# Optimization experiments

Hardware: AMD Instinct MI355X
Metric: run time of the kernel (lower is better)

The kernel has to match this reference:

```python
import jax, jax.numpy as jnp
import numpy as np

SELU_SCALE = 1.0507009873554805
SELU_ALPHA = 1.6732632423543772

def _learned_activation(x, w):
    # softmax-blended mixture of 8 activations plus a zero 'linear' branch
    p = jax.nn.softmax(w)
    sig = jax.nn.sigmoid(x)
    elu = jax.nn.elu(x)
    tanh = jnp.tanh(x)
    relu = jax.nn.relu(x)
    silu = jax.nn.silu(x)
    gelu = jax.nn.gelu(x, approximate=False)
    selu = SELU_SCALE * jnp.where(x > 0, x, SELU_ALPHA * jnp.expm1(x))
    mish = x * jnp.tanh(jax.nn.softplus(x))
    return (p[0] * sig + p[1] * elu + p[2] * tanh + p[3] * relu
            + p[4] * silu + p[5] * gelu + p[6] * selu + p[7] * mish)  # p[8]*0 (linear=0)


def setup_inputs() -> dict:
    key = jax.random.key(0)
    ks = jax.random.split(key, 10)
    B, D, H, E, M = 1024, 1024, 2048, 8, 2048
    init_units = 1024
    s = lambda fan_in: 1.0 / np.sqrt(fan_in)
    x = jax.random.normal(ks[0], (B, D), jnp.float32)
    gate_w = jax.random.normal(ks[1], (D, E), jnp.float32) * s(D)
    expert_w = jax.random.normal(ks[2], (E, D, H), jnp.float32) * s(D)
    expert_b = jnp.zeros((E, H), jnp.float32)
    conn_w1 = jax.random.normal(ks[3], (E, H, 32), jnp.float32) * s(H)
    conn_b1 = jnp.zeros((E, 32), jnp.float32)
    conn_w2 = jax.random.normal(ks[4], (E, 32, H), jnp.float32) * s(32)
    conn_b2 = jnp.zeros((E, H), jnp.float32)
    neuron_avg = jax.random.uniform(ks[5], (E, H), jnp.float32)
    # initial mask: first initial_units neurons active per expert
    neuron_mask = jnp.tile(
        jnp.concatenate([jnp.ones((init_units,), jnp.float32),
                         jnp.zeros((H - init_units,), jnp.float32)])[None, :], (E, 1))
    mem_read_w = jax.random.normal(ks[6], (H, M), jnp.float32) * s(H)
    mem_read_b = jnp.zeros((M,), jnp.float32)
    memory = jax.random.normal(ks[7], (M, H), jnp.float32) * s(M)
    act_w = jnp.ones((9,), jnp.float32)
    return {"x": x, "gate_w": gate_w, "expert_w": expert_w, "expert_b": expert_b,
            "conn_w1": conn_w1, "conn_b1": conn_b1, "conn_w2": conn_w2, "conn_b2": conn_b2,
            "neuron_avg": neuron_avg, "neuron_mask": neuron_mask,
            "mem_read_w": mem_read_w, "mem_read_b": mem_read_b,
            "memory": memory, "act_w": act_w}


def reference(x, gate_w, expert_w, expert_b, conn_w1, conn_b1, conn_w2, conn_b2,
              neuron_avg, neuron_mask, mem_read_w, mem_read_b, memory, act_w):
    # --- MoE gate over experts ---
    gate = jax.nn.softmax(x @ gate_w, axis=-1)  # [B, E]
    # --- DynamicConnectivity soft gating, per expert (from neuron_activation_avg) ---
    h1 = jax.nn.relu(jnp.einsum('eh,ehk->ek', neuron_avg, conn_w1) + conn_b1)  # [E, 32]
    conn = jax.nn.sigmoid(jnp.einsum('ek,ekh->eh', h1, conn_w2) + conn_b2)     # [E, H]
    # --- plastic dense experts: z -> gated -> masked -> relu ---
    z = jnp.einsum('bd,edh->ebh', x, expert_w) + expert_b[:, None, :]  # [E, B, H]
    a = jax.nn.relu(z * (conn * neuron_mask)[:, None, :])              # [E, B, H]
    moe_out = jnp.einsum('be,ebh->bh', gate, a)                        # [B, H]
    # --- episodic memory read (attention over memory slots) ---
    attn = jax.nn.softmax(moe_out @ mem_read_w + mem_read_b, axis=-1)  # [B, M]
    read_vec = attn @ memory                                           # [B, H]
    # --- blended learned activation on residual sum ---
    return _learned_activation(moe_out + read_vec, act_w)
```

## Files before the change

### kernel.cpp

```cpp
#include <hip/hip_runtime.h>
#include <hip/hip_bf16.h>
#include <math.h>

typedef __bf16 bf16_t;
typedef __bf16 bf16x8 __attribute__((ext_vector_type(8)));
typedef float f32x4 __attribute__((ext_vector_type(4)));

#define B_DIM 1024
#define D_DIM 1024
#define H_DIM 2048
#define E_DIM 8
#define M_DIM 2048

typedef const __attribute__((address_space(1))) unsigned int as1_uint;
typedef __attribute__((address_space(3))) unsigned int as3_uint;

__device__ __forceinline__ void gl_lds16(const void* g, void* l) {
  __builtin_amdgcn_global_load_lds((as1_uint*)g, (as3_uint*)l, 16, 0, 0);
}

#define WAITV(n) asm volatile("s_waitcnt vmcnt(" #n ")" ::: "memory")

__global__ __launch_bounds__(256) void cvt_kernel(const float* __restrict__ in,
                                                  bf16_t* __restrict__ out) {
  size_t i = ((size_t)blockIdx.x * 256 + threadIdx.x) * 8;
  float4 a = *(const float4*)&in[i];
  float4 b = *(const float4*)&in[i + 4];
  bf16x8 o;
  o[0] = (bf16_t)a.x; o[1] = (bf16_t)a.y; o[2] = (bf16_t)a.z; o[3] = (bf16_t)a.w;
  o[4] = (bf16_t)b.x; o[5] = (bf16_t)b.y; o[6] = (bf16_t)b.z; o[7] = (bf16_t)b.w;
  *(bf16x8*)&out[i] = o;
}

__global__ __launch_bounds__(256) void transpose_all(
    const float* __restrict__ ew, const float* __restrict__ mrw, const float* __restrict__ mem,
    bf16_t* __restrict__ wbT, bf16_t* __restrict__ mrT, bf16_t* __restrict__ memT) {
  __shared__ float tile[64][65];
  const int z = blockIdx.z;
  const float* in; bf16_t* out; int R, C;
  if (z < 8) {
    if (blockIdx.y >= 16) return;
    in = ew + (size_t)z * D_DIM * H_DIM; out = wbT + (size_t)z * D_DIM * H_DIM;
    R = D_DIM; C = H_DIM;
  } else if (z == 8) {
    in = mrw; out = mrT; R = H_DIM; C = M_DIM;
  } else {
    in = mem; out = memT; R = M_DIM; C = H_DIM;
  }
  int c0 = blockIdx.x * 64, r0 = blockIdx.y * 64;
  int t = threadIdx.x;
  int cq = (t & 15) * 4, rr = t >> 4;
#pragma unroll
  for (int i = 0; i < 4; ++i) {
    int r = rr + 16 * i;
    float4 v = *(const float4*)&in[(size_t)(r0 + r) * C + c0 + cq];
    tile[r][cq] = v.x; tile[r][cq + 1] = v.y; tile[r][cq + 2] = v.z; tile[r][cq + 3] = v.w;
  }
  __syncthreads();
  int r8 = (t & 7) * 8, cc = t >> 3;
#pragma unroll
  for (int i = 0; i < 2; ++i) {
    int c = cc + 32 * i;
    bf16x8 o;
#pragma unroll
    for (int j = 0; j < 8; ++j) o[j] = (bf16_t)tile[r8 + j][c];
    *(bf16x8*)&out[(size_t)(c0 + c) * R + r0 + r8] = o;
  }
}

__global__ __launch_bounds__(256) void gate_kernel(
    const float* __restrict__ x, const float* __restrict__ gw, float* __restrict__ gate_t) {
  __shared__ float red[256][8];
  int b = blockIdx.x, t = threadIdx.x;
  float acc[8] = {0.f, 0.f, 0.f, 0.f, 0.f, 0.f, 0.f, 0.f};
  for (int d = t; d < D_DIM; d += 256) {
    float xv = x[(size_t)b * D_DIM + d];
#pragma unroll
    for (int e = 0; e < 8; ++e) acc[e] += xv * gw[d * 8 + e];
  }
#pragma unroll
  for (int e = 0; e < 8; ++e) red[t][e] = acc[e];
  __syncthreads();
  for (int s = 128; s > 0; s >>= 1) {
    if (t < s) {
#pragma unroll
      for (int e = 0; e < 8; ++e) red[t][e] += red[t + s][e];
    }
    __syncthreads();
  }
  if (t == 0) {
    float m = red[0][0];
#pragma unroll
    for (int e = 1; e < 8; ++e) m = fmaxf(m, red[0][e]);
    float p[8], sum = 0.f;
#pragma unroll
    for (int e = 0; e < 8; ++e) { p[e] = expf(red[0][e] - m); sum += p[e]; }
    float inv = 1.f / sum;
#pragma unroll
    for (int e = 0; e < 8; ++e) gate_t[e * B_DIM + b] = p[e] * inv;
  }
}

__global__ __launch_bounds__(256) void conn1_kernel(
    const float* __restrict__ avg, const float* __restrict__ w1, float* __restrict__ h1p) {
  __shared__ float red[256 * 32];
  int e = blockIdx.x >> 3, c = blockIdx.x & 7, t = threadIdx.x;
  int h = c * 256 + t;
  float av = avg[e * H_DIM + h];
  const float* w1p = &w1[((size_t)e * H_DIM + h) * 32];
#pragma unroll
  for (int k = 0; k < 32; ++k) red[t * 32 + k] = av * w1p[k];
  __syncthreads();
  for (int s = 128; s > 0; s >>= 1) {
    if (t < s) {
#pragma unroll
      for (int k = 0; k < 32; ++k) red[t * 32 + k] += red[(t + s) * 32 + k];
    }
    __syncthreads();
  }
  if (t < 32) h1p[(e * 8 + c) * 32 + t] = red[t];
}

__global__ __launch_bounds__(256) void conn2_kernel(
    const float* __restrict__ h1p, const float* __restrict__ b1,
    const float* __restrict__ w2, const float* __restrict__ b2,
    const float* __restrict__ mask, float* __restrict__ conn) {
  __shared__ float h1[32];
  int e = blockIdx.x >> 3, c = blockIdx.x & 7, t = threadIdx.x;
  if (t < 32) {
    float s = 0.f;
#pragma unroll
    for (int c2 = 0; c2 < 8; ++c2) s += h1p[(e * 8 + c2) * 32 + t];
    h1[t] = fmaxf(s + b1[e * 32 + t], 0.f);
  }
  __syncthreads();
  int h = c * 256 + t;
  float s = b2[e * H_DIM + h];
#pragma unroll
  for (int k = 0; k < 32; ++k) s += h1[k] * w2[((size_t)e * 32 + k) * H_DIM + h];
  conn[e * H_DIM + h] = (1.f / (1.f + expf(-s))) * mask[e * H_DIM + h];
}

__global__ __launch_bounds__(512, 2) void expert_gemm(
    const bf16_t* __restrict__ A, const bf16_t* __restrict__ Bt,
    float* __restrict__ moe, bf16_t* __restrict__ moebf,
    const float* __restrict__ gate_t, const float* __restrict__ conn,
    const float* __restrict__ ebias) {
  __shared__ bf16_t As[2][128 * 64];
  __shared__ bf16_t Bs[8][64 * 64];

  const int wid = (blockIdx.x & 7) * 32 + (blockIdx.x >> 3);
  const int b0 = (wid & 7) * 128;
  const int n0 = (wid >> 3) * 64;

  const int t = threadIdx.x;
  const int lane = t & 63, wave = t >> 6;
  const int wmh = wave >> 2, wnq = wave & 3;
  const int lr = lane & 15, lk = (lane >> 4) * 8;
  const int csw = (lr & 7) << 3;
  const int srow = lane >> 3;
  const int scol = ((lane & 7) ^ srow) << 3;
  const size_t EB = (size_t)H_DIM * D_DIM;

  const bf16_t* Asrc = A + (size_t)(b0 + wave * 16 + srow) * D_DIM + scol;
  const bf16_t* Bsrc = Bt + (size_t)(n0 + wave * 8 + srow) * D_DIM + scol;

  auto stageA = [&](int buf, int kt) {
    gl_lds16(Asrc + (size_t)kt * 64, &As[buf][(wave * 16) * 64]);
    gl_lds16(Asrc + 8 * D_DIM + (size_t)kt * 64, &As[buf][(wave * 16 + 8) * 64]);
  };
  auto stageB = [&](int slot, int e, int kt) {
    gl_lds16(Bsrc + (size_t)e * EB + (size_t)kt * 64, &Bs[slot][(wave * 8) * 64]);
  };
  auto readB = [&](int slot, bf16x8& r0, bf16x8& r1) {
    const bf16_t* Bb = &Bs[slot][0];
    r0 = *(const bf16x8*)&Bb[(wnq * 16 + lr) * 64 + (lk ^ csw)];
    r1 = *(const bf16x8*)&Bb[(wnq * 16 + lr) * 64 + ((32 + lk) ^ csw)];
  };

  f32x4 acc[8][4];
#pragma unroll
  for (int e = 0; e < 8; ++e)
#pragma unroll
    for (int mf = 0; mf < 4; ++mf) acc[e][mf] = (f32x4){0.f, 0.f, 0.f, 0.f};

  stageA(0, 0);
#pragma unroll
  for (int s = 0; s < 5; ++s) stageB(s, s, 0);
  WAITV(3);
  __builtin_amdgcn_s_barrier();
  __builtin_amdgcn_sched_barrier(0);
  bf16x8 bc0, bc1, bn0, bn1;
  readB(0, bc0, bc1);

  for (int kt = 0; kt < 16; ++kt) {
    const int ab = kt & 1;
    const bool last = (kt == 15);
    bf16x8 af[2][4];
#pragma unroll
    for (int e = 0; e < 8; ++e) {
      if (!(last && e == 7)) readB((e + 1) & 7, bn0, bn1);
      if (e < 3) {
        stageB((e + 5) & 7, e + 5, kt);
        if (e == 0 && !last) stageA(ab ^ 1, kt + 1);
      } else if (!last) {
        stageB((e + 5) & 7, e - 3, kt + 1);
      }
      if (!last) {
        if (e < 4) { WAITV(5); } else { WAITV(3); }
      } else {
        if (e < 3)       { WAITV(3); }
        else if (e == 3) { WAITV(2); }
        else if (e == 4) { WAITV(1); }
        else             { WAITV(0); }
      }
      __builtin_amdgcn_s_barrier();
      __builtin_amdgcn_sched_barrier(0);
      if (e == 0) {
#pragma unroll
        for (int kk = 0; kk < 2; ++kk)
#pragma unroll
          for (int mf = 0; mf < 4; ++mf)
            af[kk][mf] = *(const bf16x8*)&As[ab][(wmh * 64 + mf * 16 + lr) * 64 +
                                                ((kk * 32 + lk) ^ csw)];
      }
      __builtin_amdgcn_s_setprio(1);
#pragma unroll
      for (int mf = 0; mf < 4; ++mf) {
        acc[e][mf] = __builtin_amdgcn_mfma_f32_16x16x32_bf16(af[0][mf], bc0, acc[e][mf], 0, 0, 0);
        acc[e][mf] = __builtin_amdgcn_mfma_f32_16x16x32_bf16(af[1][mf], bc1, acc[e][mf], 0, 0, 0);
      }
      __builtin_amdgcn_s_setprio(0);
      bc0 = bn0; bc1 = bn1;
    }
  }

  const int r4 = (lane >> 4) * 4;
  const int gcol = n0 + wnq * 16 + lr;
  const int growb = b0 + wmh * 64;
  f32x4 sum[4];
#pragma unroll
  for (int mf = 0; mf < 4; ++mf) sum[mf] = (f32x4){0.f, 0.f, 0.f, 0.f};
#pragma unroll
  for (int e = 0; e < 8; ++e) {
    const float cm = conn[e * H_DIM + gcol];
    const float bb = ebias[e * H_DIM + gcol];
#pragma unroll
    for (int mf = 0; mf < 4; ++mf) {
      const float4 g4 = *(const float4*)&gate_t[e * B_DIM + growb + mf * 16 + r4];
      sum[mf][0] += fmaxf((acc[e][mf][0] + bb) * cm, 0.f) * g4.x;
      sum[mf][1] += fmaxf((acc[e][mf][1] + bb) * cm, 0.f) * g4.y;
      sum[mf][2] += fmaxf((acc[e][mf][2] + bb) * cm, 0.f) * g4.z;
      sum[mf][3] += fmaxf((acc[e][mf][3] + bb) * cm, 0.f) * g4.w;
    }
  }
#pragma unroll
  for (int mf = 0; mf < 4; ++mf)
#pragma unroll
    for (int j = 0; j < 4; ++j) {
      const int grow = growb + mf * 16 + r4 + j;
      moe[(size_t)grow * H_DIM + gcol] = sum[mf][j];
      moebf[(size_t)grow * H_DIM + gcol] = (bf16_t)sum[mf][j];
    }
}

__global__ __launch_bounds__(512, 2) void gemm_sk2(
    const bf16_t* __restrict__ A, const bf16_t* __restrict__ Bt, float* __restrict__ C) {
  __shared__ bf16_t As[2][128 * 64];
  __shared__ bf16_t Bs[2][128 * 64];

  const int wid = (blockIdx.x & 7) * 32 + (blockIdx.x >> 3);
  const int ez = wid >> 7;
  const int rem = wid & 127;
  const int b0 = (rem & 7) * 128;
  const int n0 = (rem >> 3) * 128;
  const int kbase = ez << 10;

  const int t = threadIdx.x;
  const int lane = t & 63, wave = t >> 6;
  const int wm = wave >> 2, wn = wave & 3;
  const int lr = lane & 15, lk = (lane >> 4) * 8;
  const int csw = (lr & 7) << 3;
  const int srow = lane >> 3;
  const int scol = ((lane & 7) ^ srow) << 3;

  const bf16_t* Arow = A + (size_t)(b0 + srow) * 2048 + kbase + scol;
  const bf16_t* Brow = Bt + (size_t)(n0 + srow) * 2048 + kbase + scol;

  const f32x4 zv = {0.f, 0.f, 0.f, 0.f};
  f32x4 acc[4][2];
#pragma unroll
  for (int mf = 0; mf < 4; ++mf)
#pragma unroll
    for (int nf = 0; nf < 2; ++nf) acc[mf][nf] = zv;

  auto STAGE = [&](int bsel, int kt) {
    const int ko = kt << 6;
#pragma unroll
    for (int i = 0; i < 2; ++i) {
      int rb = i * 64 + wave * 8;
      gl_lds16(Arow + (size_t)rb * 2048 + ko, &As[bsel][rb * 64]);
      gl_lds16(Brow + (size_t)rb * 2048 + ko, &Bs[bsel][rb * 64]);
    }
  };

  auto COMPUTE = [&](int bsel) {
    bf16x8 bfr[2][2];
#pragma unroll
    for (int kk = 0; kk < 2; ++kk)
#pragma unroll
      for (int nf = 0; nf < 2; ++nf)
        bfr[kk][nf] = *(const bf16x8*)&Bs[bsel][(wn * 32 + nf * 16 + lr) * 64 + ((kk * 32 + lk) ^ csw)];
    __builtin_amdgcn_s_setprio(1);
#pragma unroll
    for (int mf = 0; mf < 4; ++mf) {
      bf16x8 a0 = *(const bf16x8*)&As[bsel][(wm * 64 + mf * 16 + lr) * 64 + (lk ^ csw)];
      bf16x8 a1 = *(const bf16x8*)&As[bsel][(wm * 64 + mf * 16 + lr) * 64 + ((32 + lk) ^ csw)];
#pragma unroll
      for (int nf = 0; nf < 2; ++nf)
        acc[mf][nf] = __builtin_amdgcn_mfma_f32_16x16x32_bf16(a0, bfr[0][nf], acc[mf][nf], 0, 0, 0);
#pragma unroll
      for (int nf = 0; nf < 2; ++nf)
        acc[mf][nf] = __builtin_amdgcn_mfma_f32_16x16x32_bf16(a1, bfr[1][nf], acc[mf][nf], 0, 0, 0);
    }
    __builtin_amdgcn_s_setprio(0);
  };

  STAGE(0, 0);
  __syncthreads();
  for (int kt = 0; kt < 15; ++kt) {
    STAGE((kt + 1) & 1, kt + 1);
    COMPUTE(kt & 1);
    __syncthreads();
  }
  COMPUTE(1);

  const int r4 = (lane >> 4) * 4;
#pragma unroll
  for (int mf = 0; mf < 4; ++mf) {
#pragma unroll
    for (int nf = 0; nf < 2; ++nf) {
      int gcol = n0 + wn * 32 + nf * 16 + lr;
#pragma unroll
      for (int j = 0; j < 4; ++j) {
        int grow = b0 + wm * 64 + mf * 16 + r4 + j;
        C[((size_t)ez * B_DIM + grow) * 2048 + gcol] = acc[mf][nf][j];
      }
    }
  }
}

__global__ __launch_bounds__(256) void softmax_kernel(
    const float* __restrict__ lg, const float* __restrict__ bias, bf16_t* __restrict__ attn) {
  const size_t P = (size_t)B_DIM * M_DIM;
  int b = blockIdx.x, t = threadIdx.x;
  int lane = t & 63, wave = t >> 6;
  __shared__ float rmax[4], rsum[4];
  float v[8];
  float m = -1e30f;
#pragma unroll
  for (int i = 0; i < 8; ++i) {
    size_t idx = (size_t)b * M_DIM + i * 256 + t;
    v[i] = lg[idx] + lg[P + idx] + bias[i * 256 + t];
    m = fmaxf(m, v[i]);
  }
#pragma unroll
  for (int off = 32; off >= 1; off >>= 1) m = fmaxf(m, __shfl_xor(m, off));
  if (lane == 0) rmax[wave] = m;
  __syncthreads();
  m = fmaxf(fmaxf(rmax[0], rmax[1]), fmaxf(rmax[2], rmax[3]));
  float s = 0.f;
#pragma unroll
  for (int i = 0; i < 8; ++i) {
    v[i] = __expf(v[i] - m);
    s += v[i];
  }
#pragma unroll
  for (int off = 32; off >= 1; off >>= 1) s += __shfl_xor(s, off);
  if (lane == 0) rsum[wave] = s;
  __syncthreads();
  s = rsum[0] + rsum[1] + rsum[2] + rsum[3];
  float inv = 1.f / s;
#pragma unroll
  for (int i = 0; i < 8; ++i) attn[(size_t)b * M_DIM + i * 256 + t] = (bf16_t)(v[i] * inv);
}

__global__ __launch_bounds__(256) void act_kernel(
    const float* __restrict__ rdv, const float* __restrict__ aw, float* __restrict__ out) {
  const size_t P = (size_t)B_DIM * H_DIM;
  int i = blockIdx.x * 256 + threadIdx.x;
  float w[9], m = -1e30f;
#pragma unroll
  for (int j = 0; j < 9; ++j) { w[j] = aw[j]; m = fmaxf(m, w[j]); }
  float p[9], s = 0.f;
#pragma unroll
  for (int j = 0; j < 9; ++j) { p[j] = expf(w[j] - m); s += p[j]; }
  float inv = 1.f / s;
#pragma unroll
  for (int j = 0; j < 9; ++j) p[j] *= inv;
  float4 mv = ((const float4*)out)[i];
  float4 r0 = ((const float4*)rdv)[i];
  float4 r1 = ((const float4*)(rdv + P))[i];
  float xs[4] = {mv.x + r0.x + r1.x, mv.y + r0.y + r1.y,
                 mv.z + r0.z + r1.z, mv.w + r0.w + r1.w};
  float os[4];
#pragma unroll
  for (int q = 0; q < 4; ++q) {
    float xv = xs[q];
    float enx = expf(-xv);
    float ex = expf(xv);
    float sig = 1.f / (1.f + enx);
    float em1 = expm1f(xv);
    float th = tanhf(xv);
    float rl = fmaxf(xv, 0.f);
    float si = xv * sig;
    float ge = 0.5f * xv * (1.f + erff(xv * 0.70710678118654752f));
    float se = 1.0507009873554805f * (xv > 0.f ? xv : 1.6732632423543772f * em1);
    float el = xv > 0.f ? xv : em1;
    float sp = log1pf(ex);
    float mi = xv * tanhf(sp);
    os[q] = p[0] * sig + p[1] * el + p[2] * th + p[3] * rl + p[4] * si + p[5] * ge + p[6] * se + p[7] * mi;
  }
  ((float4*)out)[i] = make_float4(os[0], os[1], os[2], os[3]);
}

extern "C" void kernel_launch(void* const* d_in, const int* in_sizes, int n_in,
                              void* d_out, int out_size, void* d_ws, size_t ws_size,
                              hipStream_t stream) {
  const float* x        = (const float*)d_in[0];
  const float* gate_w   = (const float*)d_in[1];
  const float* expert_w = (const float*)d_in[2];
  const float* expert_b = (const float*)d_in[3];
  const float* conn_w1  = (const float*)d_in[4];
  const float* conn_b1  = (const float*)d_in[5];
  const float* conn_w2  = (const float*)d_in[6];
  const float* conn_b2  = (const float*)d_in[7];
  const float* navg     = (const float*)d_in[8];
  const float* nmask    = (const float*)d_in[9];
  const float* mem_rw   = (const float*)d_in[10];
  const float* mem_rb   = (const float*)d_in[11];
  const float* memory   = (const float*)d_in[12];
  const float* act_w    = (const float*)d_in[13];
  float* out = (float*)d_out;

  char* ws = (char*)d_ws;
  bf16_t* wbT    = (bf16_t*)(ws + 0);
  bf16_t* mrT    = (bf16_t*)(ws + 33554432);
  bf16_t* memT   = (bf16_t*)(ws + 41943040);
  float*  gate_t = (float*)(ws + 50331648);
  float*  connb  = (float*)(ws + 50364416);
  bf16_t* x_bf   = (bf16_t*)(ws + 50429952);
  bf16_t* moe_bf = (bf16_t*)(ws + 52527104);
  float*  h1p    = (float*)(ws + 56721408);
  float*  logits = (float*)(ws + 0);
  bf16_t* attn   = (bf16_t*)(ws + 16777216);
  float*  readv  = (float*)(ws + 0);
  float*  moe    = out;

  cvt_kernel<<<dim3(512), 256, 0, stream>>>(x, x_bf);
  transpose_all<<<dim3(32, 32, 10), 256, 0, stream>>>(expert_w, mem_rw, memory, wbT, mrT, memT);
  gate_kernel<<<dim3(B_DIM), 256, 0, stream>>>(x, gate_w, gate_t);
  conn1_kernel<<<dim3(64), 256, 0, stream>>>(navg, conn_w1, h1p);
  conn2_kernel<<<dim3(64), 256, 0, stream>>>(h1p, conn_b1, conn_w2, conn_b2, nmask, connb);
  expert_gemm<<<dim3(256), 512, 0, stream>>>(x_bf, wbT, moe, moe_bf, gate_t, connb, expert_b);
  gemm_sk2<<<dim3(256), 512, 0, stream>>>(moe_bf, mrT, logits);
  softmax_kernel<<<dim3(B_DIM), 256, 0, stream>>>(logits, mem_rb, attn);
  gemm_sk2<<<dim3(256), 512, 0, stream>>>(attn, memT, readv);
  act_kernel<<<dim3((B_DIM * H_DIM) / (256 * 4)), 256, 0, stream>>>(readv, act_w, out);
}
```

Before: 140.0 us.

## Shrink expert GEMM tiles and raise split-K to four for memory GEMMs

```diff
diff --git a/kernel.cpp b/kernel.cpp
--- a/kernel.cpp
+++ b/kernel.cpp
@@ -141,41 +141,42 @@
   conn[e * H_DIM + h] = (1.f / (1.f + expf(-s))) * mask[e * H_DIM + h];
 }
 
-__global__ __launch_bounds__(512, 2) void expert_gemm(
+__global__ __launch_bounds__(256, 2) void expert_gemm(
     const bf16_t* __restrict__ A, const bf16_t* __restrict__ Bt,
     float* __restrict__ moe, bf16_t* __restrict__ moebf,
     const float* __restrict__ gate_t, const float* __restrict__ conn,
     const float* __restrict__ ebias) {
-  __shared__ bf16_t As[2][128 * 64];
-  __shared__ bf16_t Bs[8][64 * 64];
-
-  const int wid = (blockIdx.x & 7) * 32 + (blockIdx.x >> 3);
-  const int b0 = (wid & 7) * 128;
-  const int n0 = (wid >> 3) * 64;
+  __shared__ bf16_t As[2][64 * 64];
+  __shared__ bf16_t Bs[6][64 * 64];
+
+  const int wid = (blockIdx.x & 7) * 64 + (blockIdx.x >> 3);
+  const int b0 = (wid & 15) * 64;
+  const int n0 = (wid >> 4) * 64;
 
   const int t = threadIdx.x;
   const int lane = t & 63, wave = t >> 6;
-  const int wmh = wave >> 2, wnq = wave & 3;
   const int lr = lane & 15, lk = (lane >> 4) * 8;
   const int csw = (lr & 7) << 3;
   const int srow = lane >> 3;
   const int scol = ((lane & 7) ^ srow) << 3;
   const size_t EB = (size_t)H_DIM * D_DIM;
 
-  const bf16_t* Asrc = A + (size_t)(b0 + wave * 16 + srow) * D_DIM + scol;
+  const bf16_t* Asrc = A + (size_t)(b0 + wave * 8 + srow) * D_DIM + scol;
   const bf16_t* Bsrc = Bt + (size_t)(n0 + wave * 8 + srow) * D_DIM + scol;
 
   auto stageA = [&](int buf, int kt) {
-    gl_lds16(Asrc + (size_t)kt * 64, &As[buf][(wave * 16) * 64]);
-    gl_lds16(Asrc + 8 * D_DIM + (size_t)kt * 64, &As[buf][(wave * 16 + 8) * 64]);
+    gl_lds16(Asrc + (size_t)kt * 64, &As[buf][(wave * 8) * 64]);
+    gl_lds16(Asrc + (size_t)32 * D_DIM + (size_t)kt * 64, &As[buf][(32 + wave * 8) * 64]);
   };
   auto stageB = [&](int slot, int e, int kt) {
-    gl_lds16(Bsrc + (size_t)e * EB + (size_t)kt * 64, &Bs[slot][(wave * 8) * 64]);
+    const bf16_t* bp = Bsrc + (size_t)e * EB + (size_t)kt * 64;
+    gl_lds16(bp, &Bs[slot][(wave * 8) * 64]);
+    gl_lds16(bp + (size_t)32 * D_DIM, &Bs[slot][(32 + wave * 8) * 64]);
   };
   auto readB = [&](int slot, bf16x8& r0, bf16x8& r1) {
     const bf16_t* Bb = &Bs[slot][0];
-    r0 = *(const bf16x8*)&Bb[(wnq * 16 + lr) * 64 + (lk ^ csw)];
-    r1 = *(const bf16x8*)&Bb[(wnq * 16 + lr) * 64 + ((32 + lk) ^ csw)];
+    r0 = *(const bf16x8*)&Bb[(wave * 16 + lr) * 64 + (lk ^ csw)];
+    r1 = *(const bf16x8*)&Bb[(wave * 16 + lr) * 64 + ((32 + lk) ^ csw)];
   };
 
   f32x4 acc[8][4];
@@ -185,13 +186,16 @@
     for (int mf = 0; mf < 4; ++mf) acc[e][mf] = (f32x4){0.f, 0.f, 0.f, 0.f};
 
   stageA(0, 0);
-#pragma unroll
-  for (int s = 0; s < 5; ++s) stageB(s, s, 0);
-  WAITV(3);
+  stageB(0, 0, 0);
+  stageB(1, 1, 0);
+  stageB(2, 2, 0);
+  stageB(3, 3, 0);
+  WAITV(4);
   __builtin_amdgcn_s_barrier();
   __builtin_amdgcn_sched_barrier(0);
   bf16x8 bc0, bc1, bn0, bn1;
   readB(0, bc0, bc1);
+  int rs = 1, ss = 4;
 
   for (int kt = 0; kt < 16; ++kt) {
     const int ab = kt & 1;
@@ -199,19 +203,18 @@
     bf16x8 af[2][4];
 #pragma unroll
     for (int e = 0; e < 8; ++e) {
-      if (!(last && e == 7)) readB((e + 1) & 7, bn0, bn1);
-      if (e < 3) {
-        stageB((e + 5) & 7, e + 5, kt);
-        if (e == 0 && !last) stageA(ab ^ 1, kt + 1);
+      if (!(last && e == 7)) readB(rs, bn0, bn1);
+      if (e < 4) {
+        stageB(ss, e + 4, kt);
       } else if (!last) {
-        stageB((e + 5) & 7, e - 3, kt + 1);
+        stageB(ss, e - 4, kt + 1);
+        if (e == 4) stageA(ab ^ 1, kt + 1);
       }
       if (!last) {
-        if (e < 4) { WAITV(5); } else { WAITV(3); }
+        if (e == 4 || e == 5) { WAITV(6); } else { WAITV(4); }
       } else {
-        if (e < 3)       { WAITV(3); }
-        else if (e == 3) { WAITV(2); }
-        else if (e == 4) { WAITV(1); }
+        if (e <= 3)      { WAITV(4); }
+        else if (e == 4) { WAITV(2); }
         else             { WAITV(0); }
       }
       __builtin_amdgcn_s_barrier();
@@ -221,8 +224,7 @@
         for (int kk = 0; kk < 2; ++kk)
 #pragma unroll
           for (int mf = 0; mf < 4; ++mf)
-            af[kk][mf] = *(const bf16x8*)&As[ab][(wmh * 64 + mf * 16 + lr) * 64 +
-                                                ((kk * 32 + lk) ^ csw)];
+            af[kk][mf] = *(const bf16x8*)&As[ab][(mf * 16 + lr) * 64 + ((kk * 32 + lk) ^ csw)];
       }
       __builtin_amdgcn_s_setprio(1);
 #pragma unroll
@@ -232,12 +234,13 @@
       }
       __builtin_amdgcn_s_setprio(0);
       bc0 = bn0; bc1 = bn1;
+      rs = (rs == 5) ? 0 : rs + 1;
+      ss = (ss == 5) ? 0 : ss + 1;
     }
   }
 
   const int r4 = (lane >> 4) * 4;
-  const int gcol = n0 + wnq * 16 + lr;
-  const int growb = b0 + wmh * 64;
+  const int gcol = n0 + wave * 16 + lr;
   f32x4 sum[4];
 #pragma unroll
   for (int mf = 0; mf < 4; ++mf) sum[mf] = (f32x4){0.f, 0.f, 0.f, 0.f};
@@ -247,7 +250,7 @@
     const float bb = ebias[e * H_DIM + gcol];
 #pragma unroll
     for (int mf = 0; mf < 4; ++mf) {
-      const float4 g4 = *(const float4*)&gate_t[e * B_DIM + growb + mf * 16 + r4];
+      const float4 g4 = *(const float4*)&gate_t[e * B_DIM + b0 + mf * 16 + r4];
       sum[mf][0] += fmaxf((acc[e][mf][0] + bb) * cm, 0.f) * g4.x;
       sum[mf][1] += fmaxf((acc[e][mf][1] + bb) * cm, 0.f) * g4.y;
       sum[mf][2] += fmaxf((acc[e][mf][2] + bb) * cm, 0.f) * g4.z;
@@ -258,23 +261,23 @@
   for (int mf = 0; mf < 4; ++mf)
 #pragma unroll
     for (int j = 0; j < 4; ++j) {
-      const int grow = growb + mf * 16 + r4 + j;
+      const int grow = b0 + mf * 16 + r4 + j;
       moe[(size_t)grow * H_DIM + gcol] = sum[mf][j];
       moebf[(size_t)grow * H_DIM + gcol] = (bf16_t)sum[mf][j];
     }
 }
 
-__global__ __launch_bounds__(512, 2) void gemm_sk2(
+__global__ __launch_bounds__(512, 2) void gemm_sk4(
     const bf16_t* __restrict__ A, const bf16_t* __restrict__ Bt, float* __restrict__ C) {
   __shared__ bf16_t As[2][128 * 64];
   __shared__ bf16_t Bs[2][128 * 64];
 
-  const int wid = (blockIdx.x & 7) * 32 + (blockIdx.x >> 3);
+  const int wid = (blockIdx.x & 7) * 64 + (blockIdx.x >> 3);
   const int ez = wid >> 7;
   const int rem = wid & 127;
   const int b0 = (rem & 7) * 128;
   const int n0 = (rem >> 3) * 128;
-  const int kbase = ez << 10;
+  const int kbase = ez << 9;
 
   const int t = threadIdx.x;
   const int lane = t & 63, wave = t >> 6;
@@ -328,7 +331,7 @@
 
   STAGE(0, 0);
   __syncthreads();
-  for (int kt = 0; kt < 15; ++kt) {
+  for (int kt = 0; kt < 7; ++kt) {
     STAGE((kt + 1) & 1, kt + 1);
     COMPUTE(kt & 1);
     __syncthreads();
@@ -361,7 +364,7 @@
 #pragma unroll
   for (int i = 0; i < 8; ++i) {
     size_t idx = (size_t)b * M_DIM + i * 256 + t;
-    v[i] = lg[idx] + lg[P + idx] + bias[i * 256 + t];
+    v[i] = lg[idx] + lg[P + idx] + lg[2 * P + idx] + lg[3 * P + idx] + bias[i * 256 + t];
     m = fmaxf(m, v[i]);
   }
 #pragma unroll
@@ -401,8 +404,10 @@
   float4 mv = ((const float4*)out)[i];
   float4 r0 = ((const float4*)rdv)[i];
   float4 r1 = ((const float4*)(rdv + P))[i];
-  float xs[4] = {mv.x + r0.x + r1.x, mv.y + r0.y + r1.y,
-                 mv.z + r0.z + r1.z, mv.w + r0.w + r1.w};
+  float4 r2 = ((const float4*)(rdv + 2 * P))[i];
+  float4 r3 = ((const float4*)(rdv + 3 * P))[i];
+  float xs[4] = {mv.x + r0.x + r1.x + r2.x + r3.x, mv.y + r0.y + r1.y + r2.y + r3.y,
+                 mv.z + r0.z + r1.z + r2.z + r3.z, mv.w + r0.w + r1.w + r2.w + r3.w};
   float os[4];
 #pragma unroll
   for (int q = 0; q < 4; ++q) {
@@ -453,7 +458,7 @@
   bf16_t* moe_bf = (bf16_t*)(ws + 52527104);
   float*  h1p    = (float*)(ws + 56721408);
   float*  logits = (float*)(ws + 0);
-  bf16_t* attn   = (bf16_t*)(ws + 16777216);
+  bf16_t* attn   = (bf16_t*)(ws + 33554432);
   float*  readv  = (float*)(ws + 0);
   float*  moe    = out;
 
@@ -462,9 +467,9 @@
   gate_kernel<<<dim3(B_DIM), 256, 0, stream>>>(x, gate_w, gate_t);
   conn1_kernel<<<dim3(64), 256, 0, stream>>>(navg, conn_w1, h1p);
   conn2_kernel<<<dim3(64), 256, 0, stream>>>(h1p, conn_b1, conn_w2, conn_b2, nmask, connb);
-  expert_gemm<<<dim3(256), 512, 0, stream>>>(x_bf, wbT, moe, moe_bf, gate_t, connb, expert_b);
-  gemm_sk2<<<dim3(256), 512, 0, stream>>>(moe_bf, mrT, logits);
+  expert_gemm<<<dim3(512), 256, 0, stream>>>(x_bf, wbT, moe, moe_bf, gate_t, connb, expert_b);
+  gemm_sk4<<<dim3(512), 512, 0, stream>>>(moe_bf, mrT, logits);
   softmax_kernel<<<dim3(B_DIM), 256, 0, stream>>>(logits, mem_rb, attn);
-  gemm_sk2<<<dim3(256), 512, 0, stream>>>(attn, memT, readv);
+  gemm_sk4<<<dim3(512), 512, 0, stream>>>(attn, memT, readv);
   act_kernel<<<dim3((B_DIM * H_DIM) / (256 * 4)), 256, 0, stream>>>(readv, act_w, out);
 }
```

Result: slower. 149.9 us (+7.1%).

## Split memory GEMMs four ways along K and pair experts per pipeline step

Applied to the files above, without the earlier changes.

```diff
diff --git a/kernel.cpp b/kernel.cpp
--- a/kernel.cpp
+++ b/kernel.cpp
@@ -185,38 +185,33 @@
     for (int mf = 0; mf < 4; ++mf) acc[e][mf] = (f32x4){0.f, 0.f, 0.f, 0.f};
 
   stageA(0, 0);
-#pragma unroll
-  for (int s = 0; s < 5; ++s) stageB(s, s, 0);
-  WAITV(3);
-  __builtin_amdgcn_s_barrier();
-  __builtin_amdgcn_sched_barrier(0);
-  bf16x8 bc0, bc1, bn0, bn1;
-  readB(0, bc0, bc1);
+  stageB(0, 0, 0);
+  stageB(1, 1, 0);
+  stageB(2, 2, 0);
+  stageB(3, 3, 0);
 
   for (int kt = 0; kt < 16; ++kt) {
     const int ab = kt & 1;
     const bool last = (kt == 15);
     bf16x8 af[2][4];
 #pragma unroll
-    for (int e = 0; e < 8; ++e) {
-      if (!(last && e == 7)) readB((e + 1) & 7, bn0, bn1);
-      if (e < 3) {
-        stageB((e + 5) & 7, e + 5, kt);
-        if (e == 0 && !last) stageA(ab ^ 1, kt + 1);
+    for (int eh = 0; eh < 4; ++eh) {
+      const int e0 = eh * 2, e1 = e0 + 1;
+      if (eh < 2) {
+        stageB(e0 + 4, e0 + 4, kt);
+        stageB(e1 + 4, e1 + 4, kt);
       } else if (!last) {
-        stageB((e + 5) & 7, e - 3, kt + 1);
+        stageB(e0 - 4, e0 - 4, kt + 1);
+        stageB(e1 - 4, e1 - 4, kt + 1);
+        if (eh == 2) stageA(ab ^ 1, kt + 1);
       }
-      if (!last) {
-        if (e < 4) { WAITV(5); } else { WAITV(3); }
-      } else {
-        if (e < 3)       { WAITV(3); }
-        else if (e == 3) { WAITV(2); }
-        else if (e == 4) { WAITV(1); }
-        else             { WAITV(0); }
-      }
+      if (eh < 2)        { WAITV(4); }
+      else if (!last)    { WAITV(6); }
+      else if (eh == 2)  { WAITV(2); }
+      else               { WAITV(0); }
       __builtin_amdgcn_s_barrier();
       __builtin_amdgcn_sched_barrier(0);
-      if (e == 0) {
+      if (eh == 0) {
 #pragma unroll
         for (int kk = 0; kk < 2; ++kk)
 #pragma unroll
@@ -224,14 +219,21 @@
             af[kk][mf] = *(const bf16x8*)&As[ab][(wmh * 64 + mf * 16 + lr) * 64 +
                                                 ((kk * 32 + lk) ^ csw)];
       }
+      bf16x8 p0, p1, q0, q1;
+      readB(e0, p0, p1);
+      readB(e1, q0, q1);
       __builtin_amdgcn_s_setprio(1);
 #pragma unroll
       for (int mf = 0; mf < 4; ++mf) {
-        acc[e][mf] = __builtin_amdgcn_mfma_f32_16x16x32_bf16(af[0][mf], bc0, acc[e][mf], 0, 0, 0);
-        acc[e][mf] = __builtin_amdgcn_mfma_f32_16x16x32_bf16(af[1][mf], bc1, acc[e][mf], 0, 0, 0);
+        acc[e0][mf] = __builtin_amdgcn_mfma_f32_16x16x32_bf16(af[0][mf], p0, acc[e0][mf], 0, 0, 0);
+        acc[e0][mf] = __builtin_amdgcn_mfma_f32_16x16x32_bf16(af[1][mf], p1, acc[e0][mf], 0, 0, 0);
+      }
+#pragma unroll
+      for (int mf = 0; mf < 4; ++mf) {
+        acc[e1][mf] = __builtin_amdgcn_mfma_f32_16x16x32_bf16(af[0][mf], q0, acc[e1][mf], 0, 0, 0);
+        acc[e1][mf] = __builtin_amdgcn_mfma_f32_16x16x32_bf16(af[1][mf], q1, acc[e1][mf], 0, 0, 0);
       }
       __builtin_amdgcn_s_setprio(0);
-      bc0 = bn0; bc1 = bn1;
     }
   }
 
@@ -264,17 +266,17 @@
     }
 }
 
-__global__ __launch_bounds__(512, 2) void gemm_sk2(
+__global__ __launch_bounds__(512, 2) void gemm_sk4(
     const bf16_t* __restrict__ A, const bf16_t* __restrict__ Bt, float* __restrict__ C) {
   __shared__ bf16_t As[2][128 * 64];
   __shared__ bf16_t Bs[2][128 * 64];
 
-  const int wid = (blockIdx.x & 7) * 32 + (blockIdx.x >> 3);
+  const int wid = (blockIdx.x & 7) * 64 + (blockIdx.x >> 3);
   const int ez = wid >> 7;
   const int rem = wid & 127;
   const int b0 = (rem & 7) * 128;
   const int n0 = (rem >> 3) * 128;
-  const int kbase = ez << 10;
+  const int kbase = ez << 9;
 
   const int t = threadIdx.x;
   const int lane = t & 63, wave = t >> 6;
@@ -328,7 +330,7 @@
 
   STAGE(0, 0);
   __syncthreads();
-  for (int kt = 0; kt < 15; ++kt) {
+  for (int kt = 0; kt < 7; ++kt) {
     STAGE((kt + 1) & 1, kt + 1);
     COMPUTE(kt & 1);
     __syncthreads();
@@ -361,7 +363,7 @@
 #pragma unroll
   for (int i = 0; i < 8; ++i) {
     size_t idx = (size_t)b * M_DIM + i * 256 + t;
-    v[i] = lg[idx] + lg[P + idx] + bias[i * 256 + t];
+    v[i] = lg[idx] + lg[P + idx] + lg[2 * P + idx] + lg[3 * P + idx] + bias[i * 256 + t];
     m = fmaxf(m, v[i]);
   }
 #pragma unroll
@@ -401,8 +403,10 @@
   float4 mv = ((const float4*)out)[i];
   float4 r0 = ((const float4*)rdv)[i];
   float4 r1 = ((const float4*)(rdv + P))[i];
-  float xs[4] = {mv.x + r0.x + r1.x, mv.y + r0.y + r1.y,
-                 mv.z + r0.z + r1.z, mv.w + r0.w + r1.w};
+  float4 r2 = ((const float4*)(rdv + 2 * P))[i];
+  float4 r3 = ((const float4*)(rdv + 3 * P))[i];
+  float xs[4] = {mv.x + r0.x + r1.x + r2.x + r3.x, mv.y + r0.y + r1.y + r2.y + r3.y,
+                 mv.z + r0.z + r1.z + r2.z + r3.z, mv.w + r0.w + r1.w + r2.w + r3.w};
   float os[4];
 #pragma unroll
   for (int q = 0; q < 4; ++q) {
@@ -453,7 +457,7 @@
   bf16_t* moe_bf = (bf16_t*)(ws + 52527104);
   float*  h1p    = (float*)(ws + 56721408);
   float*  logits = (float*)(ws + 0);
-  bf16_t* attn   = (bf16_t*)(ws + 16777216);
+  bf16_t* attn   = (bf16_t*)(ws + 33554432);
   float*  readv  = (float*)(ws + 0);
   float*  moe    = out;
 
@@ -463,8 +467,8 @@
   conn1_kernel<<<dim3(64), 256, 0, stream>>>(navg, conn_w1, h1p);
   conn2_kernel<<<dim3(64), 256, 0, stream>>>(h1p, conn_b1, conn_w2, conn_b2, nmask, connb);
   expert_gemm<<<dim3(256), 512, 0, stream>>>(x_bf, wbT, moe, moe_bf, gate_t, connb, expert_b);
-  gemm_sk2<<<dim3(256), 512, 0, stream>>>(moe_bf, mrT, logits);
+  gemm_sk4<<<dim3(512), 512, 0, stream>>>(moe_bf, mrT, logits);
   softmax_kernel<<<dim3(B_DIM), 256, 0, stream>>>(logits, mem_rb, attn);
-  gemm_sk2<<<dim3(256), 512, 0, stream>>>(attn, memT, readv);
+  gemm_sk4<<<dim3(512), 512, 0, stream>>>(attn, memT, readv);
   act_kernel<<<dim3((B_DIM * H_DIM) / (256 * 4)), 256, 0, stream>>>(readv, act_w, out);
 }
```

New measurement: 134.7 us. 1.04x faster.
